# Kernel optimization log

Measured on AMD Instinct MI355X. Metric: run time of the kernel, lower is better.

The kernel has to match this reference:

```python
import jax, jax.numpy as jnp
import numpy as np

EPS_PEN = 1e-05


def _penalty(x):
    return jnp.sqrt(x + EPS_PEN)


def _warp(img, flow):
    """Bilinear warp (Resample2d): sample img at (x+u, y+v), clamped borders.
    img: (B,C,H,W), flow: (B,2,H,W) -> (B,C,H,W)."""
    B, C, H, W = img.shape
    xs = jnp.arange(W, dtype=flow.dtype)[None, None, :]  # (1,1,W)
    ys = jnp.arange(H, dtype=flow.dtype)[None, :, None]  # (1,H,1)
    x = xs + flow[:, 0]  # (B,H,W)
    y = ys + flow[:, 1]
    x0f = jnp.floor(x)
    y0f = jnp.floor(y)
    wx = x - x0f  # bilinear weights
    wy = y - y0f
    x0 = jnp.clip(x0f.astype(jnp.int32), 0, W - 1)
    x1 = jnp.clip(x0 + 1, 0, W - 1)
    y0 = jnp.clip(y0f.astype(jnp.int32), 0, H - 1)
    y1 = jnp.clip(y0 + 1, 0, H - 1)
    img_flat = img.reshape(B, C, H * W)

    def gather(yi, xi):
        idx = (yi * W + xi).reshape(B, 1, H * W)
        idx = jnp.broadcast_to(idx, (B, C, H * W))
        return jnp.take_along_axis(img_flat, idx, axis=2).reshape(B, C, H, W)

    v00 = gather(y0, x0)
    v01 = gather(y0, x1)
    v10 = gather(y1, x0)
    v11 = gather(y1, x1)
    wx = wx[:, None]  # (B,1,H,W)
    wy = wy[:, None]
    return ((1 - wy) * ((1 - wx) * v00 + wx * v01)
            + wy * ((1 - wx) * v10 + wx * v11))


def _energy(flow, img1, img2, alpha=1.0, beta=1.0):
    img2_warp = _warp(img2, flow)
    A = jnp.sum((img1 - img2_warp) ** 2, axis=1)          # (B,H,W)
    data_term = jnp.sum(_penalty(A), axis=(1, 2))          # (B,)
    # conv with kernel_dx == horizontal forward diff per channel; dy vertical
    dx = flow[:, :, :, 1:] - flow[:, :, :, :-1]            # (B,2,H,W-1)
    dy = flow[:, :, 1:, :] - flow[:, :, :-1, :]            # (B,2,H-1,W)
    Bx = jnp.pad(jnp.sum(dx ** 2, axis=1), ((0, 0), (0, 0), (0, 1)))
    By = jnp.pad(jnp.sum(dy ** 2, axis=1), ((0, 0), (0, 1), (0, 0)))
    smooth_term = jnp.sum(_penalty(Bx + By), axis=(1, 2))  # (B,)
    return alpha * data_term + beta * smooth_term


def setup_inputs() -> dict:
    key = jax.random.key(0)
    ks = jax.random.split(key, 6)
    B, H, W = 16, 448, 1024
    mean = jax.random.normal(ks[0], (B, 2, H, W), dtype=jnp.float32)
    log_var = jax.random.normal(ks[1], (B, 2, H, W), dtype=jnp.float32)
    img1 = jax.random.uniform(ks[2], (B, 3, H, W), dtype=jnp.float32)
    img2 = jax.random.uniform(ks[3], (B, 3, H, W), dtype=jnp.float32)
    target = jax.random.normal(ks[4], (B, 2, H, W), dtype=jnp.float32)
    eps = jax.random.normal(ks[5], (B, 2, H, W), dtype=jnp.float32)
    return {"mean": mean, "log_var": log_var, "img1": img1, "img2": img2,
            "target": target, "eps": eps}


def reference(mean, log_var, img1, img2, target, eps):
    # reparam: z = mean + exp(log_var/2) * eps  (eps replaces Normal(0,1).sample)
    flow_sample = mean + jnp.exp(log_var / 2.0) * eps
    elbo = _energy(flow_sample, img1, img2) - jnp.sum(log_var, axis=(1, 2, 3)) / 2.0
    mean_elbo = jnp.mean(elbo)
    # elementwise EPE: L2 norm over flow channels of (mean - target)
    epe = jnp.sqrt(jnp.sum((mean - target) ** 2, axis=1))
    mean_epe = jnp.mean(epe)
    return (mean_elbo, mean_epe)
```

## Files before the change

kernel.cpp:

```cpp
#include <hip/hip_runtime.h>

#define BB 16
#define HH 448
#define WW 1024
constexpr int HW    = HH * WW;
constexpr int NBLK  = BB * HH;
constexpr int NTHR  = 256;
constexpr long long TOTAL = (long long)BB * HW;


__global__ __launch_bounds__(NTHR) void elbo_main(
    const float* __restrict__ mean, const float* __restrict__ lvar,
    const float* __restrict__ img1, const float* __restrict__ img2,
    const float* __restrict__ target, const float* __restrict__ eps,
    float2* __restrict__ partials)
{
    constexpr int NXCD = 8, CPX = NBLK / NXCD;
    const int wg = (blockIdx.x % NXCD) * CPX + blockIdx.x / NXCD;

    const int b = wg / HH;
    const int y = wg - b * HH;
    const int t = threadIdx.x;
    const int x = t << 2;

    const int o     = b * 2 * HW + y * WW + x;
    const int ibase = b * 3 * HW;

    float se = 0.f;
    float sp = 0.f;

    const float4 m0 = *(const float4*)(mean + o);
    const float4 m1 = *(const float4*)(mean + o + HW);
    const float4 l0 = *(const float4*)(lvar + o);
    const float4 l1 = *(const float4*)(lvar + o + HW);
    const float4 e0 = *(const float4*)(eps  + o);
    const float4 e1 = *(const float4*)(eps  + o + HW);

    float u[4], v[4];
    u[0] = m0.x + __expf(0.5f * l0.x) * e0.x;
    u[1] = m0.y + __expf(0.5f * l0.y) * e0.y;
    u[2] = m0.z + __expf(0.5f * l0.z) * e0.z;
    u[3] = m0.w + __expf(0.5f * l0.w) * e0.w;
    v[0] = m1.x + __expf(0.5f * l1.x) * e1.x;
    v[1] = m1.y + __expf(0.5f * l1.y) * e1.y;
    v[2] = m1.z + __expf(0.5f * l1.z) * e1.z;
    v[3] = m1.w + __expf(0.5f * l1.w) * e1.w;

    {
        const float4 t0 = *(const float4*)(target + o);
        const float4 t1 = *(const float4*)(target + o + HW);
        float du, dv;
        du = m0.x - t0.x; dv = m1.x - t1.x; sp += sqrtf(du*du + dv*dv);
        du = m0.y - t0.y; dv = m1.y - t1.y; sp += sqrtf(du*du + dv*dv);
        du = m0.z - t0.z; dv = m1.z - t1.z; sp += sqrtf(du*du + dv*dv);
        du = m0.w - t0.w; dv = m1.w - t1.w; sp += sqrtf(du*du + dv*dv);
        se -= 0.5f * (l0.x + l0.y + l0.z + l0.w +
                      l1.x + l1.y + l1.z + l1.w);
    }

    const bool have_dn = (y + 1) < HH;
    float un[4] = {0, 0, 0, 0}, vn[4] = {0, 0, 0, 0};
    if (have_dn) {
        const int od = o + WW;
        const float4 dm0 = *(const float4*)(mean + od);
        const float4 dm1 = *(const float4*)(mean + od + HW);
        const float4 dl0 = *(const float4*)(lvar + od);
        const float4 dl1 = *(const float4*)(lvar + od + HW);
        const float4 de0 = *(const float4*)(eps  + od);
        const float4 de1 = *(const float4*)(eps  + od + HW);
        un[0] = dm0.x + __expf(0.5f * dl0.x) * de0.x;
        un[1] = dm0.y + __expf(0.5f * dl0.y) * de0.y;
        un[2] = dm0.z + __expf(0.5f * dl0.z) * de0.z;
        un[3] = dm0.w + __expf(0.5f * dl0.w) * de0.w;
        vn[0] = dm1.x + __expf(0.5f * dl1.x) * de1.x;
        vn[1] = dm1.y + __expf(0.5f * dl1.y) * de1.y;
        vn[2] = dm1.z + __expf(0.5f * dl1.z) * de1.z;
        vn[3] = dm1.w + __expf(0.5f * dl1.w) * de1.w;
    }

    float uR = __shfl_down(u[0], 1);
    float vR = __shfl_down(v[0], 1);
    if (((t & 63) == 63) && (t != NTHR - 1)) {
        const int o4 = o + 4;
        uR = mean[o4]      + __expf(0.5f * lvar[o4])      * eps[o4];
        vR = mean[o4 + HW] + __expf(0.5f * lvar[o4 + HW]) * eps[o4 + HW];
    }

    const int ro = y * WW + x;
    const float4 g0 = *(const float4*)(img1 + ibase + ro);
    const float4 g1 = *(const float4*)(img1 + ibase + HW + ro);
    const float4 g2 = *(const float4*)(img1 + ibase + 2 * HW + ro);
    const float i1c0[4] = {g0.x, g0.y, g0.z, g0.w};
    const float i1c1[4] = {g1.x, g1.y, g1.z, g1.w};
    const float i1c2[4] = {g2.x, g2.y, g2.z, g2.w};

    const float* __restrict__ p2 = img2 + ibase;

    #pragma unroll
    for (int i = 0; i < 4; ++i) {
        const float ui = u[i], vi = v[i];
        const int gx = x + i;

        float dx2 = 0.f, dy2 = 0.f;
        if (gx < WW - 1) {
            const float ur = (i < 3) ? u[i + 1] : uR;
            const float vr = (i < 3) ? v[i + 1] : vR;
            const float a = ur - ui, c = vr - vi;
            dx2 = a * a + c * c;
        }
        if (have_dn) {
            const float a = un[i] - ui, c = vn[i] - vi;
            dy2 = a * a + c * c;
        }
        se += sqrtf(dx2 + dy2 + 1e-5f);

        const float xs = (float)gx + ui;
        const float ys = (float)y  + vi;
        const float x0f = floorf(xs), y0f = floorf(ys);
        const float wx = xs - x0f,    wy = ys - y0f;
        int x0 = (int)x0f; x0 = min(max(x0, 0), WW - 1);
        const int x1 = min(x0 + 1, WW - 1);
        int yy0 = (int)y0f; yy0 = min(max(yy0, 0), HH - 1);
        const int yy1 = min(yy0 + 1, HH - 1);
        const int i00 = yy0 * WW + x0, i01 = yy0 * WW + x1;
        const int i10 = yy1 * WW + x0, i11 = yy1 * WW + x1;

        float A = 0.f;
        {
            const float v00 = p2[i00], v01 = p2[i01];
            const float v10 = p2[i10], v11 = p2[i11];
            const float top = v00 + wx * (v01 - v00);
            const float bot = v10 + wx * (v11 - v10);
            const float w   = top + wy * (bot - top);
            const float d   = i1c0[i] - w;
            A += d * d;
        }
        {
            const float v00 = p2[HW + i00], v01 = p2[HW + i01];
            const float v10 = p2[HW + i10], v11 = p2[HW + i11];
            const float top = v00 + wx * (v01 - v00);
            const float bot = v10 + wx * (v11 - v10);
            const float w   = top + wy * (bot - top);
            const float d   = i1c1[i] - w;
            A += d * d;
        }
        {
            const float v00 = p2[2*HW + i00], v01 = p2[2*HW + i01];
            const float v10 = p2[2*HW + i10], v11 = p2[2*HW + i11];
            const float top = v00 + wx * (v01 - v00);
            const float bot = v10 + wx * (v11 - v10);
            const float w   = top + wy * (bot - top);
            const float d   = i1c2[i] - w;
            A += d * d;
        }
        se += sqrtf(A + 1e-5f);
    }

    #pragma unroll
    for (int off = 32; off > 0; off >>= 1) {
        se += __shfl_down(se, off);
        sp += __shfl_down(sp, off);
    }
    __shared__ float s_e[NTHR / 64], s_p[NTHR / 64];
    const int lane = threadIdx.x & 63;
    const int wid  = threadIdx.x >> 6;
    if (lane == 0) { s_e[wid] = se; s_p[wid] = sp; }
    __syncthreads();
    if (threadIdx.x == 0) {
        float te = 0.0f, tp = 0.0f;
        #pragma unroll
        for (int i = 0; i < NTHR / 64; ++i) { te += s_e[i]; tp += s_p[i]; }
        partials[blockIdx.x] = make_float2(te, tp);
    }
}

__global__ __launch_bounds__(256) void elbo_final(
    const float2* __restrict__ partials, float* __restrict__ out)
{
    double se = 0.0, sp = 0.0;
    for (int i = threadIdx.x; i < NBLK; i += 256) {
        const float2 v = partials[i];
        se += (double)v.x;
        sp += (double)v.y;
    }
    #pragma unroll
    for (int off = 32; off > 0; off >>= 1) {
        se += __shfl_down(se, off);
        sp += __shfl_down(sp, off);
    }
    __shared__ double s_e[4], s_p[4];
    const int lane = threadIdx.x & 63;
    const int wid  = threadIdx.x >> 6;
    if (lane == 0) { s_e[wid] = se; s_p[wid] = sp; }
    __syncthreads();
    if (threadIdx.x == 0) {
        double te = 0.0, tp = 0.0;
        #pragma unroll
        for (int i = 0; i < 4; ++i) { te += s_e[i]; tp += s_p[i]; }
        out[0] = (float)(te / (double)BB);
        out[1] = (float)(tp / (double)TOTAL);
    }
}

extern "C" void kernel_launch(void* const* d_in, const int* in_sizes, int n_in,
                              void* d_out, int out_size, void* d_ws, size_t ws_size,
                              hipStream_t stream) {
    const float* mean   = (const float*)d_in[0];
    const float* logvar = (const float*)d_in[1];
    const float* img1   = (const float*)d_in[2];
    const float* img2   = (const float*)d_in[3];
    const float* target = (const float*)d_in[4];
    const float* eps    = (const float*)d_in[5];
    float* out = (float*)d_out;
    float2* partials = (float2*)d_ws;

    elbo_main<<<NBLK, NTHR, 0, stream>>>(mean, logvar, img1, img2, target, eps, partials);
    elbo_final<<<1, 256, 0, stream>>>(partials, out);
}
```

Baseline: 477.5 us.

## Switch to strided per-pixel mapping with software-pipelined scalar loads

```diff
diff --git a/kernel.cpp b/kernel.cpp
--- a/kernel.cpp
+++ b/kernel.cpp
@@ -8,6 +8,12 @@
 constexpr int NTHR  = 256;
 constexpr long long TOTAL = (long long)BB * HW;
 
+
+struct FlowRaw {
+    float m0, m1, l0, l1, e0, e1;
+    float dm0, dm1, dl0, dl1, de0, de1;
+    float t0, t1;
+};
 
 __global__ __launch_bounds__(NTHR) void elbo_main(
     const float* __restrict__ mean, const float* __restrict__ lvar,
@@ -21,101 +27,72 @@
     const int b = wg / HH;
     const int y = wg - b * HH;
     const int t = threadIdx.x;
-    const int x = t << 2;
 
-    const int o     = b * 2 * HW + y * WW + x;
+    const int fbase = b * 2 * HW + y * WW;
     const int ibase = b * 3 * HW;
+    const bool have_dn = (y + 1) < HH;
+
+    const float* __restrict__ p2c0 = img2 + ibase;
+    const float* __restrict__ p2c1 = img2 + ibase + HW;
+    const float* __restrict__ p2c2 = img2 + ibase + 2 * HW;
 
     float se = 0.f;
     float sp = 0.f;
 
-    const float4 m0 = *(const float4*)(mean + o);
-    const float4 m1 = *(const float4*)(mean + o + HW);
-    const float4 l0 = *(const float4*)(lvar + o);
-    const float4 l1 = *(const float4*)(lvar + o + HW);
-    const float4 e0 = *(const float4*)(eps  + o);
-    const float4 e1 = *(const float4*)(eps  + o + HW);
+    auto load_raw = [&](int k, FlowRaw& r) {
+        const int o = fbase + (k << 8) + t;
+        r.m0 = mean[o];   r.m1 = mean[o + HW];
+        r.l0 = lvar[o];   r.l1 = lvar[o + HW];
+        r.e0 = eps[o];    r.e1 = eps[o + HW];
+        r.t0 = target[o]; r.t1 = target[o + HW];
+        if (have_dn) {
+            r.dm0 = mean[o + WW]; r.dm1 = mean[o + WW + HW];
+            r.dl0 = lvar[o + WW]; r.dl1 = lvar[o + WW + HW];
+            r.de0 = eps[o + WW];  r.de1 = eps[o + WW + HW];
+        } else {
+            r.dm0 = r.dm1 = r.dl0 = r.dl1 = r.de0 = r.de1 = 0.f;
+        }
+    };
 
-    float u[4], v[4];
-    u[0] = m0.x + __expf(0.5f * l0.x) * e0.x;
-    u[1] = m0.y + __expf(0.5f * l0.y) * e0.y;
-    u[2] = m0.z + __expf(0.5f * l0.z) * e0.z;
-    u[3] = m0.w + __expf(0.5f * l0.w) * e0.w;
-    v[0] = m1.x + __expf(0.5f * l1.x) * e1.x;
-    v[1] = m1.y + __expf(0.5f * l1.y) * e1.y;
-    v[2] = m1.z + __expf(0.5f * l1.z) * e1.z;
-    v[3] = m1.w + __expf(0.5f * l1.w) * e1.w;
-
-    {
-        const float4 t0 = *(const float4*)(target + o);
-        const float4 t1 = *(const float4*)(target + o + HW);
-        float du, dv;
-        du = m0.x - t0.x; dv = m1.x - t1.x; sp += sqrtf(du*du + dv*dv);
-        du = m0.y - t0.y; dv = m1.y - t1.y; sp += sqrtf(du*du + dv*dv);
-        du = m0.z - t0.z; dv = m1.z - t1.z; sp += sqrtf(du*du + dv*dv);
-        du = m0.w - t0.w; dv = m1.w - t1.w; sp += sqrtf(du*du + dv*dv);
-        se -= 0.5f * (l0.x + l0.y + l0.z + l0.w +
-                      l1.x + l1.y + l1.z + l1.w);
-    }
-
-    const bool have_dn = (y + 1) < HH;
-    float un[4] = {0, 0, 0, 0}, vn[4] = {0, 0, 0, 0};
-    if (have_dn) {
-        const int od = o + WW;
-        const float4 dm0 = *(const float4*)(mean + od);
-        const float4 dm1 = *(const float4*)(mean + od + HW);
-        const float4 dl0 = *(const float4*)(lvar + od);
-        const float4 dl1 = *(const float4*)(lvar + od + HW);
-        const float4 de0 = *(const float4*)(eps  + od);
-        const float4 de1 = *(const float4*)(eps  + od + HW);
-        un[0] = dm0.x + __expf(0.5f * dl0.x) * de0.x;
-        un[1] = dm0.y + __expf(0.5f * dl0.y) * de0.y;
-        un[2] = dm0.z + __expf(0.5f * dl0.z) * de0.z;
-        un[3] = dm0.w + __expf(0.5f * dl0.w) * de0.w;
-        vn[0] = dm1.x + __expf(0.5f * dl1.x) * de1.x;
-        vn[1] = dm1.y + __expf(0.5f * dl1.y) * de1.y;
-        vn[2] = dm1.z + __expf(0.5f * dl1.z) * de1.z;
-        vn[3] = dm1.w + __expf(0.5f * dl1.w) * de1.w;
-    }
-
-    float uR = __shfl_down(u[0], 1);
-    float vR = __shfl_down(v[0], 1);
-    if (((t & 63) == 63) && (t != NTHR - 1)) {
-        const int o4 = o + 4;
-        uR = mean[o4]      + __expf(0.5f * lvar[o4])      * eps[o4];
-        vR = mean[o4 + HW] + __expf(0.5f * lvar[o4 + HW]) * eps[o4 + HW];
-    }
-
-    const int ro = y * WW + x;
-    const float4 g0 = *(const float4*)(img1 + ibase + ro);
-    const float4 g1 = *(const float4*)(img1 + ibase + HW + ro);
-    const float4 g2 = *(const float4*)(img1 + ibase + 2 * HW + ro);
-    const float i1c0[4] = {g0.x, g0.y, g0.z, g0.w};
-    const float i1c1[4] = {g1.x, g1.y, g1.z, g1.w};
-    const float i1c2[4] = {g2.x, g2.y, g2.z, g2.w};
-
-    const float* __restrict__ p2 = img2 + ibase;
+    FlowRaw cur, nxt;
+    load_raw(0, cur);
 
     #pragma unroll
-    for (int i = 0; i < 4; ++i) {
-        const float ui = u[i], vi = v[i];
-        const int gx = x + i;
+    for (int k = 0; k < 4; ++k) {
+        if (k < 3) load_raw(k + 1, nxt);
+
+        const int x = (k << 8) + t;
+        const int o = fbase + x;
+
+        const float u = cur.m0 + __expf(0.5f * cur.l0) * cur.e0;
+        const float v = cur.m1 + __expf(0.5f * cur.l1) * cur.e1;
+        float un = 0.f, vn = 0.f;
+        if (have_dn) {
+            un = cur.dm0 + __expf(0.5f * cur.dl0) * cur.de0;
+            vn = cur.dm1 + __expf(0.5f * cur.dl1) * cur.de1;
+        }
+
+        {
+            const float du = cur.m0 - cur.t0, dv = cur.m1 - cur.t1;
+            sp += sqrtf(du * du + dv * dv);
+        }
+        se -= 0.5f * (cur.l0 + cur.l1);
+
+        float uR = __shfl_down(u, 1);
+        float vR = __shfl_down(v, 1);
+        if (((t & 63) == 63) && (x + 1 < WW)) {
+            const int o1 = o + 1;
+            uR = mean[o1]      + __expf(0.5f * lvar[o1])      * eps[o1];
+            vR = mean[o1 + HW] + __expf(0.5f * lvar[o1 + HW]) * eps[o1 + HW];
+        }
 
         float dx2 = 0.f, dy2 = 0.f;
-        if (gx < WW - 1) {
-            const float ur = (i < 3) ? u[i + 1] : uR;
-            const float vr = (i < 3) ? v[i + 1] : vR;
-            const float a = ur - ui, c = vr - vi;
-            dx2 = a * a + c * c;
-        }
-        if (have_dn) {
-            const float a = un[i] - ui, c = vn[i] - vi;
-            dy2 = a * a + c * c;
-        }
+        if (x < WW - 1) { const float a = uR - u, c = vR - v; dx2 = a * a + c * c; }
+        if (have_dn)    { const float a = un - u, c = vn - v; dy2 = a * a + c * c; }
         se += sqrtf(dx2 + dy2 + 1e-5f);
 
-        const float xs = (float)gx + ui;
-        const float ys = (float)y  + vi;
+        const float xs = (float)x + u;
+        const float ys = (float)y + v;
         const float x0f = floorf(xs), y0f = floorf(ys);
         const float wx = xs - x0f,    wy = ys - y0f;
         int x0 = (int)x0f; x0 = min(max(x0, 0), WW - 1);
@@ -125,35 +102,37 @@
         const int i00 = yy0 * WW + x0, i01 = yy0 * WW + x1;
         const int i10 = yy1 * WW + x0, i11 = yy1 * WW + x1;
 
+        const int ro = y * WW + x;
+        const float i1a = img1[ibase + ro];
+        const float i1b = img1[ibase + HW + ro];
+        const float i1c = img1[ibase + 2 * HW + ro];
+
+        const float a00 = p2c0[i00], a01 = p2c0[i01], a10 = p2c0[i10], a11 = p2c0[i11];
+        const float b00 = p2c1[i00], b01 = p2c1[i01], b10 = p2c1[i10], b11 = p2c1[i11];
+        const float c00 = p2c2[i00], c01 = p2c2[i01], c10 = p2c2[i10], c11 = p2c2[i11];
+
         float A = 0.f;
         {
-            const float v00 = p2[i00], v01 = p2[i01];
-            const float v10 = p2[i10], v11 = p2[i11];
-            const float top = v00 + wx * (v01 - v00);
-            const float bot = v10 + wx * (v11 - v10);
+            const float top = a00 + wx * (a01 - a00);
+            const float bot = a10 + wx * (a11 - a10);
             const float w   = top + wy * (bot - top);
-            const float d   = i1c0[i] - w;
-            A += d * d;
+            const float d   = i1a - w;  A += d * d;
         }
         {
-            const float v00 = p2[HW + i00], v01 = p2[HW + i01];
-            const float v10 = p2[HW + i10], v11 = p2[HW + i11];
-            const float top = v00 + wx * (v01 - v00);
-            const float bot = v10 + wx * (v11 - v10);
+            const float top = b00 + wx * (b01 - b00);
+            const float bot = b10 + wx * (b11 - b10);
             const float w   = top + wy * (bot - top);
-            const float d   = i1c1[i] - w;
-            A += d * d;
+            const float d   = i1b - w;  A += d * d;
         }
         {
-            const float v00 = p2[2*HW + i00], v01 = p2[2*HW + i01];
-            const float v10 = p2[2*HW + i10], v11 = p2[2*HW + i11];
-            const float top = v00 + wx * (v01 - v00);
-            const float bot = v10 + wx * (v11 - v10);
+            const float top = c00 + wx * (c01 - c00);
+            const float bot = c10 + wx * (c11 - c10);
             const float w   = top + wy * (bot - top);
-            const float d   = i1c2[i] - w;
-            A += d * d;
+            const float d   = i1c - w;  A += d * d;
         }
         se += sqrtf(A + 1e-5f);
+
+        if (k < 3) cur = nxt;
     }
 
     #pragma unroll
```

Measured after the change: 404.5 us. 1.18x faster.
